# Performance work log

Hardware: AMD Instinct MI355X
Metric: run time of the kernel (lower is better)

Reference implementation:

```python
import jax, jax.numpy as jnp
import numpy as np

R, S, M, K = 512, 48, 4096, 16
RADIUS = 4.0 * 0.025
DIMS = [511, 256, 256, 256, 3]


def posenc(x, n_freqs):
    freqs = 2.0 ** jnp.arange(n_freqs, dtype=x.dtype)
    xf = x[..., None, :] * freqs[:, None]            # [..., F, C]
    sc = jnp.stack([jnp.sin(xf), jnp.cos(xf)], -2)   # [..., F, 2, C]
    return jnp.concatenate([x, sc.reshape(x.shape[:-1] + (-1,))], -1)


def ball_query(q, p, radius, k):
    # pytorch3d-style: first k points (by index order) within radius.
    # dists are squared distances, 0 for padding; neighbors are 0 for padding; idx -1 for padding.
    d2 = jnp.sum((q[:, None, :] - p[None, :, :]) ** 2, -1)    # [Nq, M]
    m = p.shape[0]
    order = jnp.where(d2 < radius * radius, jnp.arange(m), m)
    neg, idx = jax.lax.top_k(-order, k)                        # k smallest valid indices
    valid = neg > -m
    dists = jnp.where(valid, jnp.take_along_axis(d2, idx, axis=1), 0.0)
    nbrs = jnp.where(valid[..., None], p[idx], 0.0)
    return dists, jnp.where(valid, idx, -1), nbrs


def setup_inputs() -> dict:
    key = jax.random.key(0)
    ks = jax.random.split(key, 16)
    inp = {
        "points": jax.random.uniform(ks[0], (R, S, 3), jnp.float32),
        "normals": jax.random.normal(ks[1], (R * S, 3), jnp.float32),
        "view_dirs": jax.random.normal(ks[2], (R * S, 3), jnp.float32),
        "feature_vectors": jax.random.normal(ks[3], (R * S, 256), jnp.float32),
        "indices": 0,
        "physical_particles": jax.random.uniform(ks[4], (M, 3), jnp.float32),
        "rays": jax.random.normal(ks[5], (R, 6), jnp.float32),
        "ro": jax.random.normal(ks[6], (1, 3), jnp.float32),
    }
    for l in range(4):
        scale = (2.0 / DIMS[l + 1]) ** 0.5
        inp[f"W{l}"] = jax.random.normal(ks[7 + l], (DIMS[l + 1], DIMS[l]), jnp.float32) * scale
        inp[f"b{l}"] = jnp.zeros((DIMS[l + 1],), jnp.float32)
    return inp


def reference(points, normals, view_dirs, feature_vectors, indices, physical_particles,
              rays, ro, W0, b0, W1, b1, W2, b2, W3, b3):
    q = points.reshape(-1, 3)                                     # [R*S, 3]
    dists, idx, nbrs = ball_query(q, physical_particles, RADIUS, K)
    dists = dists.reshape(R, S, K)
    nbrs = nbrs.reshape(R, S, K, 3)
    nn_mask = dists != 0                                          # padded entries have dist 0
    num_nn = nn_mask.sum(-1, keepdims=True)                       # [R, S, 1]

    hit_pos_emb = posenc(q, 10)                                   # [R*S, 63]
    hit_dir_emb = jnp.repeat(posenc(rays[:, 3:], 4), S, axis=0)   # [R*S, 27]

    # smoothing_position (exclude_ray=True)
    dn = jnp.linalg.norm(nbrs - points[:, :, None, :], axis=-1)   # [R, S, K]
    w = jnp.maximum(1.0 - (dn / RADIUS) ** 3, 0.0)
    density = w.sum(-1, keepdims=True)                            # [R, S, 1]
    smoothed = (w[..., None] * nbrs).sum(-2) / (density + 1e-12)  # [R, S, 3]

    sp = smoothed.reshape(-1, 3)
    dirs = sp - ro
    dirs = dirs / jnp.linalg.norm(dirs, axis=-1, keepdims=True)

    density_emb = posenc(density.reshape(-1, 1), 4)               # [R*S, 9]
    smoothed_pos_emb = posenc(sp, 10)                             # [R*S, 63]

    # masked variance of neighbor offsets
    diff = jnp.where(nn_mask[..., None], nbrs - points[:, :, None, :], 0.0)
    mean = diff.sum(-2) / (num_nn + 1e-12)
    var = jnp.where(nn_mask[..., None], (diff - mean[:, :, None, :]) ** 2, 0.0).sum(-2) / (num_nn + 1e-12)
    var_emb = posenc(var.reshape(-1, 3), 10)                      # [R*S, 63]

    x = jnp.concatenate([hit_pos_emb, density_emb, smoothed_pos_emb, var_emb,
                         hit_dir_emb, posenc(dirs, 4), normals, feature_vectors], -1)  # [R*S, 511]

    for Wl, bl in ((W0, b0), (W1, b1), (W2, b2)):
        x = jax.nn.relu(x @ Wl.T + bl)
    return jax.nn.sigmoid(x @ W3.T + b3)
```

## Files before the change

kernel.cpp:

```cpp
#include <hip/hip_runtime.h>

typedef _Float16 f16;
typedef f16 f16x8 __attribute__((ext_vector_type(8)));
typedef float f32x4 __attribute__((ext_vector_type(4)));
typedef unsigned short u16;

__device__ __forceinline__ void glds16(const void* g, void* l) {
  __builtin_amdgcn_global_load_lds(
      (const __attribute__((address_space(1))) unsigned*)g,
      (__attribute__((address_space(3))) unsigned*)l, 16, 0, 0);
}


struct FT {
  u16 v[256];
  static constexpr u16 enc(int s, int f, int k) {
    return (u16)(s | (f << 5) | (k << 9));
  }
  constexpr void p3(int base, int F, int src) {
    v[base + 0] = enc(src + 0, 0, 0);
    v[base + 1] = enc(src + 1, 0, 0);
    v[base + 2] = enc(src + 2, 0, 0);
    for (int f = 0; f < F; ++f)
      for (int r = 0; r < 6; ++r) {
        int comp = (r < 3) ? r : r - 3;
        v[base + 3 + f * 6 + r] = enc(src + comp, f, (r < 3) ? 1 : 2);
      }
  }
  constexpr void p1(int base, int F, int src) {
    v[base] = enc(src, 0, 0);
    for (int f = 0; f < F; ++f) {
      v[base + 1 + 2 * f] = enc(src, f, 1);
      v[base + 2 + 2 * f] = enc(src, f, 2);
    }
  }
  constexpr FT() : v{} {
    p3(0, 10, 0);
    p1(63, 4, 3);
    p3(72, 10, 4);
    p3(135, 10, 7);
    p3(198, 4, 10);
    p3(225, 4, 13);
    v[252] = enc(16, 0, 0);
    v[253] = enc(17, 0, 0);
    v[254] = enc(18, 0, 0);
    v[255] = enc(0, 0, 3);
  }
};
__constant__ FT ftab = FT();

__device__ float4 g_sorted[4096];
__device__ int    g_cellStart[1001];

__global__ __launch_bounds__(1024) void build_grid(const float* __restrict__ parts)
{
  __shared__ int cnt[1000];
  __shared__ int pos[1000];
  __shared__ int wpre[125];
  const int tid = threadIdx.x;
  for (int j = tid; j < 1000; j += 1024) cnt[j] = 0;
  __syncthreads();

  float px[4], py[4], pz[4];
  int cd[4];
  #pragma unroll
  for (int t = 0; t < 4; ++t) {
    int i = tid + t * 1024;
    float x = parts[3 * i], y = parts[3 * i + 1], z = parts[3 * i + 2];
    int cx = min(max((int)(x * 10.0f), 0), 9);
    int cy = min(max((int)(y * 10.0f), 0), 9);
    int cz = min(max((int)(z * 10.0f), 0), 9);
    cd[t] = (cz * 10 + cy) * 10 + cx;
    px[t] = x; py[t] = y; pz[t] = z;
    atomicAdd(&cnt[cd[t]], 1);
  }
  __syncthreads();

  if (tid < 125) {
    int s = 0;
    #pragma unroll
    for (int k = 0; k < 8; ++k) s += cnt[tid * 8 + k];
    wpre[tid] = s;
  }
  __syncthreads();
  if (tid == 0) {
    int s = 0;
    for (int c = 0; c < 125; ++c) { int t = wpre[c]; wpre[c] = s; s += t; }
  }
  __syncthreads();
  if (tid < 125) {
    int run = wpre[tid];
    #pragma unroll
    for (int k = 0; k < 8; ++k) {
      int c = tid * 8 + k;
      int n = cnt[c];
      pos[c] = run;
      g_cellStart[c] = run;
      run += n;
    }
  }
  if (tid == 0) g_cellStart[1000] = 4096;
  __syncthreads();

  #pragma unroll
  for (int t = 0; t < 4; ++t) {
    int p = atomicAdd(&pos[cd[t]], 1);
    g_sorted[p] = make_float4(px[t], py[t], pz[t], __int_as_float(tid + t * 1024));
  }
}

__global__ __launch_bounds__(256) void prep_weights(
    const float* __restrict__ W0, const float* __restrict__ W1,
    const float* __restrict__ W2,
    f16* __restrict__ w0f, f16* __restrict__ w1f, f16* __restrict__ w2f)
{
  int i = blockIdx.x * 256 + threadIdx.x;
  float v; f16* pf; int n, c;
  if (i < 131072) {
    n = i >> 9; c = i & 511;
    v = (c < 255) ? W0[n * 511 + c] : ((c == 255) ? 0.0f : W0[n * 511 + (c - 1)]);
    pf = w0f;
  } else if (i < 196608) {
    int j = i - 131072; n = j >> 8; c = j & 255; v = W1[j]; pf = w1f;
  } else {
    int j = i - 196608; n = j >> 8; c = j & 255; v = W2[j]; pf = w2f;
  }
  int kt = c >> 5, g = (c >> 3) & 3, jj = c & 7;
  int u = n * 4 + (g ^ ((n >> 1) & 3));
  pf[kt * 8192 + u * 8 + jj] = (f16)v;
}

#define MAXCH 5

__global__ __launch_bounds__(256) void feat_kernel(
    const float* __restrict__ points, const float* __restrict__ normals,
    const float* __restrict__ parts, const float* __restrict__ rays,
    const float* __restrict__ ro, f16* __restrict__ Xf)
{
  __shared__ float sdata[4][20];

  const int tid = threadIdx.x;
  const int lane = tid & 63, wv = tid >> 6;
  const int q = blockIdx.x * 4 + wv;
  const float qx = points[3 * q], qy = points[3 * q + 1], qz = points[3 * q + 2];
  const float RQ = 0.1f * 0.1f;

  int nAcc = 0;
  float sdx = 0, sdy = 0, sdz = 0;
  float s2x = 0, s2y = 0, s2z = 0;
  float sw = 0, swx = 0, swy = 0, swz = 0;

  const int cqx = min(max((int)(qx * 10.0f), 0), 9);
  const int cqy = min(max((int)(qy * 10.0f), 0), 9);
  const int cqz = min(max((int)(qz * 10.0f), 0), 9);

  int st_l = 0, cn_l = 0;
  if (lane < 9) {
    int dz = lane / 3, dy = lane - dz * 3;
    int cz = cqz - 1 + dz, cy = cqy - 1 + dy;
    if ((unsigned)cz <= 9u && (unsigned)cy <= 9u) {
      int x0 = max(cqx - 1, 0), x1 = min(cqx + 1, 9);
      int rb = (cz * 10 + cy) * 10;
      st_l = g_cellStart[rb + x0];
      cn_l = g_cellStart[rb + x1 + 1] - st_l;
    }
  }

  int pk[9], bk[9];
  int run = 0;
  #pragma unroll
  for (int k = 0; k < 9; ++k) {
    int stk = __builtin_amdgcn_readlane(st_l, k);
    int cnk = __builtin_amdgcn_readlane(cn_l, k);
    pk[k] = run;
    bk[k] = stk - run;
    run += cnk;
  }
  const int C = run;
  const bool fb = (C > MAXCH * 64);

  if (!fb) {
    float4 sv[MAXCH];
    int iv[MAXCH];
    unsigned long long hm[MAXCH];
    #pragma unroll
    for (int ch = 0; ch < MAXCH; ++ch) {
      if (ch * 64 < C) {
        int s = ch * 64 + lane;
        int g = bk[0];
        #pragma unroll
        for (int k = 1; k < 9; ++k) g = (s >= pk[k]) ? bk[k] : g;
        float4 pt = g_sorted[min(g + s, 4095)];
        if (s >= C) {
          pt.x = 1e9f; pt.y = 1e9f; pt.z = 1e9f;
          pt.w = __int_as_float(0x7fffffff);
        }
        sv[ch] = pt;
        iv[ch] = __float_as_int(pt.w);
        float ex = pt.x - qx, ey = pt.y - qy, ez = pt.z - qz;
        float d2 = __fadd_rn(__fadd_rn(__fmul_rn(ex, ex), __fmul_rn(ey, ey)),
                             __fmul_rn(ez, ez));
        hm[ch] = __ballot(d2 < RQ);
      } else {
        hm[ch] = 0ULL;
      }
    }

    int N = 0;
    #pragma unroll
    for (int ch = 0; ch < MAXCH; ++ch) N += __popcll(hm[ch]);

    int thr = 0x7fffffff;
    if (N > 16) {
      int lo = 0, hi = 4095;
      while (lo < hi) {
        int mid = (lo + hi) >> 1;
        int c = 0;
        #pragma unroll
        for (int ch = 0; ch < MAXCH; ++ch)
          if (ch * 64 < C)
            c += __popcll(hm[ch] & __ballot(iv[ch] <= mid));
        if (c >= 16) hi = mid; else lo = mid + 1;
      }
      thr = lo;
    }

    #pragma unroll
    for (int ch = 0; ch < MAXCH; ++ch) {
      if (ch * 64 < C) {
        float4 pt = sv[ch];
        float ex = pt.x - qx, ey = pt.y - qy, ez = pt.z - qz;
        float d2 = __fadd_rn(__fadd_rn(__fmul_rn(ex, ex), __fmul_rn(ey, ey)),
                             __fmul_rn(ez, ez));
        if (d2 < RQ && iv[ch] <= thr) {
          nAcc++;
          sdx += ex; sdy += ey; sdz += ez;
          s2x += ex * ex; s2y += ey * ey; s2z += ez * ez;
          float dn = sqrtf(d2);
          float t = dn * 10.0f;
          float w = fmaxf(1.0f - t * t * t, 0.0f);
          sw += w; swx += w * pt.x; swy += w * pt.y; swz += w * pt.z;
        }
      }
    }
  } else {
    int total = 0;
    for (int jr = 0; jr < 64; ++jr) {
      int pi = jr * 64 + lane;
      float x = parts[3 * pi], y = parts[3 * pi + 1], z = parts[3 * pi + 2];
      float ex = x - qx, ey = y - qy, ez = z - qz;
      float d2 = __fadd_rn(__fadd_rn(__fmul_rn(ex, ex), __fmul_rn(ey, ey)),
                           __fmul_rn(ez, ez));
      bool hit = d2 < RQ;
      unsigned long long m = __ballot(hit);
      int pos = __builtin_amdgcn_mbcnt_hi((unsigned)(m >> 32),
                __builtin_amdgcn_mbcnt_lo((unsigned)m, 0u));
      if (hit && (total + pos < 16)) {
        nAcc++;
        sdx += ex; sdy += ey; sdz += ez;
        s2x += ex * ex; s2y += ey * ey; s2z += ez * ez;
        float dn = sqrtf(d2);
        float t = dn * 10.0f;
        float w = fmaxf(1.0f - t * t * t, 0.0f);
        sw += w; swx += w * x; swy += w * y; swz += w * z;
      }
      total += __popcll(m);
      if (total >= 16) break;
    }
  }

  #define WRED(x) { _Pragma("unroll") for (int o = 32; o; o >>= 1) x += __shfl_xor(x, o, 64); }
  float fn = (float)nAcc;
  WRED(fn); WRED(sdx); WRED(sdy); WRED(sdz);
  WRED(s2x); WRED(s2y); WRED(s2z);
  WRED(sw); WRED(swx); WRED(swy); WRED(swz);
  #undef WRED

  float tq = sqrtf(qx * qx + qy * qy + qz * qz) * 10.0f;
  float wpad = fmaxf(1.0f - tq * tq * tq, 0.0f);
  float density = sw + (16.0f - fn) * wpad;
  float invd = 1.0f / (density + 1e-12f);
  float spx = swx * invd, spy = swy * invd, spz = swz * invd;

  float invn = 1.0f / (fn + 1e-12f);
  float mx = sdx * invn, my = sdy * invn, mz = sdz * invn;
  float vx = fmaxf((s2x - 2.0f * mx * sdx + fn * mx * mx) * invn, 0.0f);
  float vy = fmaxf((s2y - 2.0f * my * sdy + fn * my * my) * invn, 0.0f);
  float vz = fmaxf((s2z - 2.0f * mz * sdz + fn * mz * mz) * invn, 0.0f);

  float dxx = spx - ro[0], dyy = spy - ro[1], dzz = spz - ro[2];
  float il = 1.0f / sqrtf(dxx * dxx + dyy * dyy + dzz * dzz);

  if (lane == 0) {
    float* s = sdata[wv];
    s[0] = qx; s[1] = qy; s[2] = qz; s[3] = density;
    s[4] = spx; s[5] = spy; s[6] = spz;
    s[7] = vx; s[8] = vy; s[9] = vz;
    int r = q / 48;
    s[10] = rays[6 * r + 3]; s[11] = rays[6 * r + 4]; s[12] = rays[6 * r + 5];
    s[13] = dxx * il; s[14] = dyy * il; s[15] = dzz * il;
    s[16] = normals[3 * q]; s[17] = normals[3 * q + 1]; s[18] = normals[3 * q + 2];
  }
  __syncthreads();

  const int b = q / 48, m48 = q % 48;
  const size_t base = (size_t)b * 12288;
  #pragma unroll
  for (int it = 0; it < 4; ++it) {
    int c = it * 64 + lane;
    int e = ftab.v[c];
    float sv_ = sdata[wv][e & 31];
    float arg = sv_ * (float)(1 << ((e >> 5) & 15));
    float sn, cs;
    sincosf(arg, &sn, &cs);
    int kind = e >> 9;
    float val = (kind == 0) ? sv_ : (kind == 1 ? sn : (kind == 2 ? cs : 0.0f));
    int kt = c >> 5, g = (c >> 3) & 3, j = c & 7;
    int u = m48 * 4 + (g ^ ((m48 >> 1) & 3));
    Xf[base + kt * 1536 + u * 8 + j] = (f16)val;
  }
}

__global__ __launch_bounds__(256, 2) void fused_mlp(
    const f16* __restrict__ Xf, const float* __restrict__ fvec,
    const f16* __restrict__ w0f, const f16* __restrict__ w1f,
    const f16* __restrict__ w2f,
    const float* __restrict__ b0, const float* __restrict__ b1,
    const float* __restrict__ b2,
    const float* __restrict__ W3, const float* __restrict__ b3,
    float* __restrict__ out)
{
  extern __shared__ char lds[];
  f16* As = (f16*)lds;
  f16* H2 = (f16*)lds;
  f16* Hf = (f16*)(lds + 49152);
  float* w3s = (float*)(lds + 28672);

  const int tid = threadIdx.x, lane = tid & 63, wn = tid >> 6;
  const int l15 = lane & 15, l4 = lane >> 4;
  const int blk = blockIdx.x;

  f32x4 acc[3][4];

  const f16* Xft = Xf + (size_t)blk * 12288;

  int uB[4];
  #pragma unroll
  for (int j = 0; j < 4; ++j) {
    int n = wn * 64 + j * 16 + l15;
    uB[j] = n * 4 + (l4 ^ ((n >> 1) & 3));
  }
  int uA[3];
  #pragma unroll
  for (int i = 0; i < 3; ++i) {
    int m = i * 16 + l15;
    uA[i] = m * 4 + (l4 ^ ((m >> 1) & 3));
  }

  auto zacc = [&]() {
    #pragma unroll
    for (int i = 0; i < 3; ++i)
      #pragma unroll
      for (int j = 0; j < 4; ++j) acc[i][j] = (f32x4){0, 0, 0, 0};
  };
  auto loadB = [&](const f16* wf, int kt, f16x8* bf) {
    #pragma unroll
    for (int j = 0; j < 4; ++j)
      bf[j] = *(const f16x8*)(wf + kt * 8192 + uB[j] * 8);
  };
  auto mfmas = [&](f16x8* af, f16x8* bf) {
    #pragma unroll
    for (int i = 0; i < 3; ++i)
      #pragma unroll
      for (int j = 0; j < 4; ++j)
        acc[i][j] = __builtin_amdgcn_mfma_f32_16x16x32_f16(af[i], bf[j], acc[i][j], 0, 0, 0);
  };
  auto epilogue = [&](const float* bias_, f16* Hdst) {
    float bv[4];
    #pragma unroll
    for (int j = 0; j < 4; ++j) bv[j] = bias_[wn * 64 + j * 16 + l15];
    #pragma unroll
    for (int i = 0; i < 3; ++i) {
      #pragma unroll
      for (int r = 0; r < 4; ++r) {
        int m = i * 16 + l4 * 4 + r;
        #pragma unroll
        for (int j = 0; j < 4; ++j) {
          int n = wn * 64 + j * 16 + l15;
          float v = fmaxf(acc[i][j][r] + bv[j], 0.0f);
          int u = m * 32 + ((n >> 3) ^ ((m >> 1) & 7));
          Hdst[u * 8 + (n & 7)] = (f16)v;
        }
      }
    }
  };

  #pragma unroll
  for (int r = 0; r < 6; ++r)
    glds16(Xft + r * 2048 + tid * 8, As + r * 2048 + tid * 8);
  if (tid < 192) {
    int m = tid >> 2, g = tid & 3;
    int u = m * 4 + (g ^ ((m >> 1) & 3));
    #pragma unroll
    for (int kf = 0; kf < 8; ++kf) {
      const float* src = fvec + (size_t)(blk * 48 + m) * 256 + kf * 32 + g * 8;
      float4 v0 = ((const float4*)src)[0];
      float4 v1 = ((const float4*)src)[1];
      f16 hs[8] = {(f16)v0.x, (f16)v0.y, (f16)v0.z, (f16)v0.w,
                   (f16)v1.x, (f16)v1.y, (f16)v1.z, (f16)v1.w};
      *(uint4*)(As + (8 + kf) * 1536 + u * 8) = *(uint4*)hs;
    }
  }
  __syncthreads();

  zacc();
  {
    f16x8 bf[4], bfn[4];
    loadB(w0f, 0, bf);
    #pragma unroll
    for (int kt = 0; kt < 16; ++kt) {
      if (kt < 15) loadB(w0f, kt + 1, bfn);
      f16x8 af[3];
      #pragma unroll
      for (int i = 0; i < 3; ++i)
        af[i] = *(const f16x8*)(As + kt * 1536 + uA[i] * 8);
      mfmas(af, bf);
      #pragma unroll
      for (int j = 0; j < 4; ++j) bf[j] = bfn[j];
    }
  }
  epilogue(b0, Hf);
  __syncthreads();

  zacc();
  {
    f16x8 bf[4], bfn[4];
    loadB(w1f, 0, bf);
    #pragma unroll
    for (int kt = 0; kt < 8; ++kt) {
      if (kt < 7) loadB(w1f, kt + 1, bfn);
      f16x8 af[3];
      #pragma unroll
      for (int i = 0; i < 3; ++i) {
        int m = i * 16 + l15;
        int g = kt * 4 + l4;
        int u = m * 32 + (g ^ ((m >> 1) & 7));
        af[i] = *(const f16x8*)(Hf + u * 8);
      }
      mfmas(af, bf);
      #pragma unroll
      for (int j = 0; j < 4; ++j) bf[j] = bfn[j];
    }
  }
  epilogue(b1, H2);
  __syncthreads();

  zacc();
  {
    f16x8 bf[4], bfn[4];
    loadB(w2f, 0, bf);
    #pragma unroll
    for (int kt = 0; kt < 8; ++kt) {
      if (kt < 7) loadB(w2f, kt + 1, bfn);
      f16x8 af[3];
      #pragma unroll
      for (int i = 0; i < 3; ++i) {
        int m = i * 16 + l15;
        int g = kt * 4 + l4;
        int u = m * 32 + (g ^ ((m >> 1) & 7));
        af[i] = *(const f16x8*)(H2 + u * 8);
      }
      mfmas(af, bf);
      #pragma unroll
      for (int j = 0; j < 4; ++j) bf[j] = bfn[j];
    }
  }
  epilogue(b2, Hf);

  __syncthreads();
  for (int i = tid; i < 768; i += 256) w3s[i] = W3[i];
  __syncthreads();

  const float B30 = b3[0], B31 = b3[1], B32 = b3[2];
  #pragma unroll 1
  for (int rr = 0; rr < 12; ++rr) {
    int m = wn * 12 + rr;
    int g = lane >> 1, j0 = (lane & 1) * 4;
    int u = m * 32 + (g ^ ((m >> 1) & 7));
    uint2 pk = *(const uint2*)(Hf + u * 8 + j0);
    f16 h4[4];
    *(uint2*)h4 = pk;
    float h0 = (float)h4[0], h1 = (float)h4[1], h2 = (float)h4[2], h3 = (float)h4[3];
    int kc = lane * 4;
    float4 wa = *(const float4*)(w3s + kc);
    float4 wb = *(const float4*)(w3s + 256 + kc);
    float4 wc = *(const float4*)(w3s + 512 + kc);
    float p0 = fmaf(h3, wa.w, fmaf(h2, wa.z, fmaf(h1, wa.y, h0 * wa.x)));
    float p1 = fmaf(h3, wb.w, fmaf(h2, wb.z, fmaf(h1, wb.y, h0 * wb.x)));
    float p2 = fmaf(h3, wc.w, fmaf(h2, wc.z, fmaf(h1, wc.y, h0 * wc.x)));
    #pragma unroll
    for (int o = 32; o; o >>= 1) {
      p0 += __shfl_xor(p0, o, 64);
      p1 += __shfl_xor(p1, o, 64);
      p2 += __shfl_xor(p2, o, 64);
    }
    if (lane == 0) {
      size_t ro_ = (size_t)(blk * 48 + m) * 3;
      out[ro_ + 0] = 1.0f / (1.0f + expf(-(p0 + B30)));
      out[ro_ + 1] = 1.0f / (1.0f + expf(-(p1 + B31)));
      out[ro_ + 2] = 1.0f / (1.0f + expf(-(p2 + B32)));
    }
  }
}

extern "C" void kernel_launch(void* const* d_in, const int* in_sizes, int n_in,
                              void* d_out, int out_size, void* d_ws, size_t ws_size,
                              hipStream_t stream) {
  const float* points  = (const float*)d_in[0];
  const float* normals = (const float*)d_in[1];
  const float* fvec    = (const float*)d_in[3];
  const float* parts   = (const float*)d_in[5];
  const float* rays    = (const float*)d_in[6];
  const float* ro      = (const float*)d_in[7];
  const float* W0 = (const float*)d_in[8];
  const float* b0 = (const float*)d_in[9];
  const float* W1 = (const float*)d_in[10];
  const float* b1 = (const float*)d_in[11];
  const float* W2 = (const float*)d_in[12];
  const float* b2 = (const float*)d_in[13];
  const float* W3 = (const float*)d_in[14];
  const float* b3 = (const float*)d_in[15];

  char* ws = (char*)d_ws;
  f16* Xf  = (f16*)(ws);
  f16* w0f = (f16*)(ws + 12582912);
  f16* w1f = (f16*)(ws + 12845056);
  f16* w2f = (f16*)(ws + 12976128);
  float* out = (float*)d_out;

  (void)hipFuncSetAttribute((const void*)fused_mlp,
                            hipFuncAttributeMaxDynamicSharedMemorySize, 73728);

  build_grid<<<1, 1024, 0, stream>>>(parts);
  prep_weights<<<1024, 256, 0, stream>>>(W0, W1, W2, w0f, w1f, w2f);
  feat_kernel<<<6144, 256, 0, stream>>>(points, normals, parts, rays, ro, Xf);
  fused_mlp<<<512, 256, 73728, stream>>>(Xf, fvec, w0f, w1f, w2f,
                                         b0, b1, b2, W3, b3, out);
}
```

Before: 173.5 us.

## Use 8 waves per MLP block with deeper B prefetch and reduced LDS

The fused MLP kernel now runs 512 threads per block, so each wave covers 32 output columns instead of 64. This halves the per-wave accumulators, which leaves room for a 3-deep register ring of weight fragments and double-buffered A fragments that overlap loads with MFMAs. The LDS layout is compacted from 72KB to 51KB so more blocks can be resident, and an extra barrier is added before the first epilogue because Hf now aliases the input tile. In exchange, each wave does fewer MFMAs per A load, so A-fragment LDS reads are duplicated across twice as many waves.

```diff
diff --git a/kernel.cpp b/kernel.cpp
--- a/kernel.cpp
+++ b/kernel.cpp
@@ -321,7 +321,7 @@
   }
 }
 
-__global__ __launch_bounds__(256, 2) void fused_mlp(
+__global__ __launch_bounds__(512, 4) void fused_mlp(
     const f16* __restrict__ Xf, const float* __restrict__ fvec,
     const f16* __restrict__ w0f, const f16* __restrict__ w1f,
     const f16* __restrict__ w2f,
@@ -332,22 +332,24 @@
 {
   extern __shared__ char lds[];
   f16* As = (f16*)lds;
-  f16* H2 = (f16*)lds;
-  f16* Hf = (f16*)(lds + 49152);
-  float* w3s = (float*)(lds + 28672);
+  f16* Hf = (f16*)lds;
+  f16* H2 = (f16*)(lds + 24576);
+  float* w3s = (float*)(lds + 49152);
 
   const int tid = threadIdx.x, lane = tid & 63, wn = tid >> 6;
   const int l15 = lane & 15, l4 = lane >> 4;
   const int blk = blockIdx.x;
 
-  f32x4 acc[3][4];
+  f32x4 acc[3][2];
+  f16x8 bq[3][2];
+  f16x8 af[2][3];
 
   const f16* Xft = Xf + (size_t)blk * 12288;
 
-  int uB[4];
-  #pragma unroll
-  for (int j = 0; j < 4; ++j) {
-    int n = wn * 64 + j * 16 + l15;
+  int uB[2];
+  #pragma unroll
+  for (int j = 0; j < 2; ++j) {
+    int n = wn * 32 + j * 16 + l15;
     uB[j] = n * 4 + (l4 ^ ((n >> 1) & 3));
   }
   int uA[3];
@@ -361,32 +363,46 @@
     #pragma unroll
     for (int i = 0; i < 3; ++i)
       #pragma unroll
-      for (int j = 0; j < 4; ++j) acc[i][j] = (f32x4){0, 0, 0, 0};
+      for (int j = 0; j < 2; ++j) acc[i][j] = (f32x4){0, 0, 0, 0};
   };
   auto loadB = [&](const f16* wf, int kt, f16x8* bf) {
     #pragma unroll
-    for (int j = 0; j < 4; ++j)
+    for (int j = 0; j < 2; ++j)
       bf[j] = *(const f16x8*)(wf + kt * 8192 + uB[j] * 8);
   };
-  auto mfmas = [&](f16x8* af, f16x8* bf) {
+  auto loadA0 = [&](int kt, f16x8* a3) {
+    #pragma unroll
+    for (int i = 0; i < 3; ++i)
+      a3[i] = *(const f16x8*)(As + kt * 1536 + uA[i] * 8);
+  };
+  auto loadAH = [&](const f16* Hsrc, int kt, f16x8* a3) {
+    #pragma unroll
+    for (int i = 0; i < 3; ++i) {
+      int m = i * 16 + l15;
+      int g = kt * 4 + l4;
+      int u = m * 32 + (g ^ ((m >> 1) & 7));
+      a3[i] = *(const f16x8*)(Hsrc + u * 8);
+    }
+  };
+  auto mfmas = [&](f16x8* a3, f16x8* b2) {
     #pragma unroll
     for (int i = 0; i < 3; ++i)
       #pragma unroll
-      for (int j = 0; j < 4; ++j)
-        acc[i][j] = __builtin_amdgcn_mfma_f32_16x16x32_f16(af[i], bf[j], acc[i][j], 0, 0, 0);
+      for (int j = 0; j < 2; ++j)
+        acc[i][j] = __builtin_amdgcn_mfma_f32_16x16x32_f16(a3[i], b2[j], acc[i][j], 0, 0, 0);
   };
   auto epilogue = [&](const float* bias_, f16* Hdst) {
-    float bv[4];
-    #pragma unroll
-    for (int j = 0; j < 4; ++j) bv[j] = bias_[wn * 64 + j * 16 + l15];
+    float bv[2];
+    #pragma unroll
+    for (int j = 0; j < 2; ++j) bv[j] = bias_[wn * 32 + j * 16 + l15];
     #pragma unroll
     for (int i = 0; i < 3; ++i) {
       #pragma unroll
       for (int r = 0; r < 4; ++r) {
         int m = i * 16 + l4 * 4 + r;
         #pragma unroll
-        for (int j = 0; j < 4; ++j) {
-          int n = wn * 64 + j * 16 + l15;
+        for (int j = 0; j < 2; ++j) {
+          int n = wn * 32 + j * 16 + l15;
           float v = fmaxf(acc[i][j][r] + bv[j], 0.0f);
           int u = m * 32 + ((n >> 3) ^ ((m >> 1) & 7));
           Hdst[u * 8 + (n & 7)] = (f16)v;
@@ -396,13 +412,14 @@
   };
 
   #pragma unroll
-  for (int r = 0; r < 6; ++r)
-    glds16(Xft + r * 2048 + tid * 8, As + r * 2048 + tid * 8);
-  if (tid < 192) {
-    int m = tid >> 2, g = tid & 3;
+  for (int r = 0; r < 3; ++r)
+    glds16(Xft + r * 4096 + tid * 8, As + r * 4096 + tid * 8);
+  if (tid < 384) {
+    int m = tid >> 3, sub = tid & 7, g = sub & 3, kh = sub >> 2;
     int u = m * 4 + (g ^ ((m >> 1) & 3));
     #pragma unroll
-    for (int kf = 0; kf < 8; ++kf) {
+    for (int t = 0; t < 4; ++t) {
+      int kf = kh * 4 + t;
       const float* src = fvec + (size_t)(blk * 48 + m) * 256 + kf * 32 + g * 8;
       float4 v0 = ((const float4*)src)[0];
       float4 v1 = ((const float4*)src)[1];
@@ -411,80 +428,55 @@
       *(uint4*)(As + (8 + kf) * 1536 + u * 8) = *(uint4*)hs;
     }
   }
+  loadB(w0f, 0, bq[0]);
+  loadB(w0f, 1, bq[1]);
   __syncthreads();
 
   zacc();
-  {
-    f16x8 bf[4], bfn[4];
-    loadB(w0f, 0, bf);
-    #pragma unroll
-    for (int kt = 0; kt < 16; ++kt) {
-      if (kt < 15) loadB(w0f, kt + 1, bfn);
-      f16x8 af[3];
-      #pragma unroll
-      for (int i = 0; i < 3; ++i)
-        af[i] = *(const f16x8*)(As + kt * 1536 + uA[i] * 8);
-      mfmas(af, bf);
-      #pragma unroll
-      for (int j = 0; j < 4; ++j) bf[j] = bfn[j];
-    }
-  }
+  loadA0(0, af[0]);
+  #pragma unroll
+  for (int kt = 0; kt < 16; ++kt) {
+    if (kt < 14) loadB(w0f, kt + 2, bq[(kt + 2) % 3]);
+    if (kt < 15) loadA0(kt + 1, af[(kt + 1) & 1]);
+    mfmas(af[kt & 1], bq[kt % 3]);
+  }
+  loadB(w1f, 0, bq[0]);
+  loadB(w1f, 1, bq[1]);
+  __syncthreads();
   epilogue(b0, Hf);
   __syncthreads();
 
   zacc();
-  {
-    f16x8 bf[4], bfn[4];
-    loadB(w1f, 0, bf);
-    #pragma unroll
-    for (int kt = 0; kt < 8; ++kt) {
-      if (kt < 7) loadB(w1f, kt + 1, bfn);
-      f16x8 af[3];
-      #pragma unroll
-      for (int i = 0; i < 3; ++i) {
-        int m = i * 16 + l15;
-        int g = kt * 4 + l4;
-        int u = m * 32 + (g ^ ((m >> 1) & 7));
-        af[i] = *(const f16x8*)(Hf + u * 8);
-      }
-      mfmas(af, bf);
-      #pragma unroll
-      for (int j = 0; j < 4; ++j) bf[j] = bfn[j];
-    }
-  }
+  loadAH(Hf, 0, af[0]);
+  #pragma unroll
+  for (int kt = 0; kt < 8; ++kt) {
+    if (kt < 6) loadB(w1f, kt + 2, bq[(kt + 2) % 3]);
+    if (kt < 7) loadAH(Hf, kt + 1, af[(kt + 1) & 1]);
+    mfmas(af[kt & 1], bq[kt % 3]);
+  }
+  loadB(w2f, 0, bq[0]);
+  loadB(w2f, 1, bq[1]);
   epilogue(b1, H2);
   __syncthreads();
 
   zacc();
-  {
-    f16x8 bf[4], bfn[4];
-    loadB(w2f, 0, bf);
-    #pragma unroll
-    for (int kt = 0; kt < 8; ++kt) {
-      if (kt < 7) loadB(w2f, kt + 1, bfn);
-      f16x8 af[3];
-      #pragma unroll
-      for (int i = 0; i < 3; ++i) {
-        int m = i * 16 + l15;
-        int g = kt * 4 + l4;
-        int u = m * 32 + (g ^ ((m >> 1) & 7));
-        af[i] = *(const f16x8*)(H2 + u * 8);
-      }
-      mfmas(af, bf);
-      #pragma unroll
-      for (int j = 0; j < 4; ++j) bf[j] = bfn[j];
-    }
+  loadAH(H2, 0, af[0]);
+  #pragma unroll
+  for (int kt = 0; kt < 8; ++kt) {
+    if (kt < 6) loadB(w2f, kt + 2, bq[(kt + 2) % 3]);
+    if (kt < 7) loadAH(H2, kt + 1, af[(kt + 1) & 1]);
+    mfmas(af[kt & 1], bq[kt % 3]);
   }
   epilogue(b2, Hf);
-
-  __syncthreads();
-  for (int i = tid; i < 768; i += 256) w3s[i] = W3[i];
+  __syncthreads();
+
+  for (int i = tid; i < 768; i += 512) w3s[i] = W3[i];
   __syncthreads();
 
   const float B30 = b3[0], B31 = b3[1], B32 = b3[2];
   #pragma unroll 1
-  for (int rr = 0; rr < 12; ++rr) {
-    int m = wn * 12 + rr;
+  for (int rr = 0; rr < 6; ++rr) {
+    int m = wn * 6 + rr;
     int g = lane >> 1, j0 = (lane & 1) * 4;
     int u = m * 32 + (g ^ ((m >> 1) & 7));
     uint2 pk = *(const uint2*)(Hf + u * 8 + j0);
@@ -539,11 +531,11 @@
   float* out = (float*)d_out;
 
   (void)hipFuncSetAttribute((const void*)fused_mlp,
-                            hipFuncAttributeMaxDynamicSharedMemorySize, 73728);
+                            hipFuncAttributeMaxDynamicSharedMemorySize, 52224);
 
   build_grid<<<1, 1024, 0, stream>>>(parts);
   prep_weights<<<1024, 256, 0, stream>>>(W0, W1, W2, w0f, w1f, w2f);
   feat_kernel<<<6144, 256, 0, stream>>>(points, normals, parts, rays, ro, Xf);
-  fused_mlp<<<512, 256, 73728, stream>>>(Xf, fvec, w0f, w1f, w2f,
+  fused_mlp<<<512, 512, 52224, stream>>>(Xf, fvec, w0f, w1f, w2f,
                                          b0, b1, b2, W3, b3, out);
 }
```

Measured after the change: 157.1 us. 1.1x faster.
